# Performance work log

Measured on AMD Instinct MI355X. Metric: run time of the kernel, lower is better.

The kernel has to match this reference:

```python
import jax, jax.numpy as jnp
import numpy as np

D_MODEL, D_K, D_V = 1024, 128, 128
B, S = 4, 4096

def setup_inputs() -> dict:
    key = jax.random.key(0)
    ks = jax.random.split(key, 9)
    sq = 1.0 / np.sqrt(D_MODEL)
    return {
        "q": jax.random.normal(ks[0], (B, S, D_MODEL), jnp.float32),
        "k": jax.random.normal(ks[1], (B, S, D_MODEL), jnp.float32),
        "v": jax.random.normal(ks[2], (B, S, D_MODEL), jnp.float32),
        "wq": jax.random.uniform(ks[3], (D_MODEL, D_K), jnp.float32, -sq, sq),
        "bq": jax.random.uniform(ks[4], (D_K,), jnp.float32, -sq, sq),
        "wk": jax.random.uniform(ks[5], (D_MODEL, D_K), jnp.float32, -sq, sq),
        "bk": jax.random.uniform(ks[6], (D_K,), jnp.float32, -sq, sq),
        "wv": jax.random.uniform(ks[7], (D_MODEL, D_V), jnp.float32, -sq, sq),
        "bv": jax.random.uniform(ks[8], (D_V,), jnp.float32, -sq, sq),
    }

def reference(q, k, v, wq, bq, wk, bk, wv, bv):
    scale = 1.0 / jnp.sqrt(jnp.asarray(D_K, q.dtype))
    qp = q @ wq + bq            # [B,S,Dk]
    kp = k @ wk + bk            # [B,S,Dk]
    vp = v @ wv + bv            # [B,S,Dv]
    scores = jnp.einsum('bqd,bkd->bqk', qp, kp) * scale  # [B,S,S]
    attn = jax.nn.softmax(scores, axis=-1)
    return jnp.einsum('bqk,bkd->bqd', attn, vp)          # [B,S,Dv]
```

## Files before the change

### kernel.cpp

```cpp
#include <hip/hip_runtime.h>

#define DM 1024
#define DK 128
#define SEQ 4096
#define NB 4
#define NSPLIT 4
#define KSPAN (SEQ / NSPLIT)
#define NQT (SEQ / 128)

typedef float f32x4 __attribute__((ext_vector_type(4)));
typedef float f32x16 __attribute__((ext_vector_type(16)));
typedef __bf16 bf16x8 __attribute__((ext_vector_type(8)));
typedef unsigned short u16x8 __attribute__((ext_vector_type(8)));
typedef unsigned short u16x4 __attribute__((ext_vector_type(4)));

__device__ __forceinline__ unsigned short f2bf(float f) {
    unsigned int u = __builtin_bit_cast(unsigned int, f);
    u += 0x7fffu + ((u >> 16) & 1u);
    return (unsigned short)(u >> 16);
}
__device__ __forceinline__ float bf2f(unsigned short h) {
    unsigned int u = ((unsigned int)h) << 16;
    return __builtin_bit_cast(float, u);
}
__device__ __forceinline__ f32x4 mfma16(u16x8 a, u16x8 b, f32x4 c) {
    return __builtin_amdgcn_mfma_f32_16x16x32_bf16(
        __builtin_bit_cast(bf16x8, a), __builtin_bit_cast(bf16x8, b), c, 0, 0, 0);
}
__device__ __forceinline__ f32x16 mfma32(u16x8 a, u16x8 b, f32x16 c) {
    return __builtin_amdgcn_mfma_f32_32x32x16_bf16(
        __builtin_bit_cast(bf16x8, a), __builtin_bit_cast(bf16x8, b), c, 0, 0, 0);
}

__global__ __launch_bounds__(256) void wt_kernel(
        const float* __restrict__ wq, const float* __restrict__ wk,
        const float* __restrict__ wv, unsigned short* __restrict__ wT) {
    __shared__ unsigned short T[64 * 72];
    const int kt = blockIdx.x, dt = blockIdx.y, mat = blockIdx.z;
    const float* src = (mat == 0) ? wq : (mat == 1 ? wk : wv);
    const int tid = threadIdx.x;
    const int rb = tid >> 4, c4 = (tid & 15) * 4;
    float4 x[4];
#pragma unroll
    for (int i = 0; i < 4; i++)
        x[i] = *(const float4*)&src[(size_t)(kt * 64 + i * 16 + rb) * DK + dt * 64 + c4];
#pragma unroll
    for (int i = 0; i < 4; i++) {
        const int row = i * 16 + rb;
        T[(c4 + 0) * 72 + row] = f2bf(x[i].x);
        T[(c4 + 1) * 72 + row] = f2bf(x[i].y);
        T[(c4 + 2) * 72 + row] = f2bf(x[i].z);
        T[(c4 + 3) * 72 + row] = f2bf(x[i].w);
    }
    __syncthreads();
    const int dl = tid >> 2, ks0 = (tid & 3) * 16;
    unsigned short* dst = wT + (size_t)mat * DM * DK + (size_t)(dt * 64 + dl) * DM + kt * 64 + ks0;
#pragma unroll
    for (int j = 0; j < 2; j++)
        *(u16x8*)&dst[8 * j] = *(const u16x8*)&T[dl * 72 + ks0 + 8 * j];
}

__global__ __launch_bounds__(256)
__attribute__((amdgpu_waves_per_eu(3, 3)))
void proj_kernel(
        const float* __restrict__ qin, const float* __restrict__ kin,
        const float* __restrict__ vin, const unsigned short* __restrict__ wT,
        const float* __restrict__ bq, const float* __restrict__ bk,
        const float* __restrict__ bv,
        unsigned short* __restrict__ qp, unsigned short* __restrict__ kp,
        unsigned short* __restrict__ vpT) {
    __shared__ unsigned short Xs[64 * 136];
    __shared__ unsigned short Ws[128 * 136];
    const int y = blockIdx.y;
    const float* X = (y == 0) ? qin : (y == 1 ? kin : vin);
    const unsigned short* WTm = wT + (size_t)y * (DM * DK);
    const float* bias = (y == 0) ? bq : (y == 1 ? bk : bv);

    const int tid = threadIdx.x;
    const int w = tid >> 6, lane = tid & 63, l16 = lane & 15, quad = lane >> 4;
    const int t0 = blockIdx.x * 64;
    const int xr = tid >> 5, xc = (tid & 31) * 4;
    const int wr = tid >> 4, wc = (tid & 15) * 8;

    f32x4 zero = {0.f, 0.f, 0.f, 0.f};
    f32x4 acc[4][2];
#pragma unroll
    for (int mf = 0; mf < 4; mf++)
#pragma unroll
        for (int nf = 0; nf < 2; nf++) acc[mf][nf] = zero;

    float4 xv[8];
    uint4 wv[8];
#pragma unroll
    for (int i = 0; i < 8; i++) {
        xv[i] = *(const float4*)&X[(size_t)(t0 + i * 8 + xr) * DM + xc];
        wv[i] = *(const uint4*)&WTm[(size_t)(i * 16 + wr) * DM + wc];
    }

    for (int k0 = 0; k0 < DM; k0 += 128) {
        __syncthreads();
#pragma unroll
        for (int i = 0; i < 8; i++) {
            u16x4 p;
            p[0] = f2bf(xv[i].x); p[1] = f2bf(xv[i].y);
            p[2] = f2bf(xv[i].z); p[3] = f2bf(xv[i].w);
            *(u16x4*)&Xs[(i * 8 + xr) * 136 + xc] = p;
            *(u16x8*)&Ws[(i * 16 + wr) * 136 + wc] = __builtin_bit_cast(u16x8, wv[i]);
        }
        __syncthreads();
        if (k0 + 128 < DM) {
#pragma unroll
            for (int i = 0; i < 8; i++) {
                xv[i] = *(const float4*)&X[(size_t)(t0 + i * 8 + xr) * DM + (k0 + 128) + xc];
                wv[i] = *(const uint4*)&WTm[(size_t)(i * 16 + wr) * DM + (k0 + 128) + wc];
            }
        }
#pragma unroll
        for (int ks = 0; ks < 4; ks++) {
            u16x8 av[4], bvf[2];
#pragma unroll
            for (int mf = 0; mf < 4; mf++)
                av[mf] = *(const u16x8*)&Xs[(l16 + 16 * mf) * 136 + ks * 32 + quad * 8];
#pragma unroll
            for (int nf = 0; nf < 2; nf++)
                bvf[nf] = *(const u16x8*)&Ws[(l16 + 32 * w + 16 * nf) * 136 + ks * 32 + quad * 8];
#pragma unroll
            for (int mf = 0; mf < 4; mf++)
#pragma unroll
                for (int nf = 0; nf < 2; nf++)
                    acc[mf][nf] = mfma16(av[mf], bvf[nf], acc[mf][nf]);
        }
    }
    if (y < 2) {
        unsigned short* outp = y ? kp : qp;
#pragma unroll
        for (int nf = 0; nf < 2; nf++) {
            const int n = l16 + 32 * w + 16 * nf;
            const float bb = bias[n];
#pragma unroll
            for (int mf = 0; mf < 4; mf++)
#pragma unroll
                for (int r = 0; r < 4; r++)
                    outp[(size_t)(t0 + 16 * mf + quad * 4 + r) * DK + n] = f2bf(acc[mf][nf][r] + bb);
        }
    } else {
        __syncthreads();
        unsigned short* Tb = Ws;
#pragma unroll
        for (int nf = 0; nf < 2; nf++) {
            const int d = l16 + 32 * w + 16 * nf;
            const float bb = bias[d];
#pragma unroll
            for (int mf = 0; mf < 4; mf++)
#pragma unroll
                for (int r = 0; r < 4; r++)
                    Tb[d * 72 + 16 * mf + quad * 4 + r] = f2bf(acc[mf][nf][r] + bb);
        }
        __syncthreads();
        const int d2 = tid >> 1, ts = (tid & 1) * 32;
        const int b2 = t0 >> 12, tl0 = t0 & (SEQ - 1);
#pragma unroll
        for (int j = 0; j < 4; j++)
            *(u16x8*)&vpT[((size_t)(b2 * DK + d2)) * SEQ + tl0 + ts + 8 * j] =
                *(const u16x8*)&Tb[d2 * 72 + ts + 8 * j];
    }
}

__global__ __launch_bounds__(256)
__attribute__((amdgpu_waves_per_eu(2, 2)))
void attn_part_kernel(
        const unsigned short* __restrict__ qp, const unsigned short* __restrict__ kp,
        const unsigned short* __restrict__ vpT,
        unsigned short* __restrict__ Opart, float* __restrict__ Lw) {
    __shared__ unsigned short Ks[64 * 136];
    __shared__ unsigned short Vs[128 * 72];

    const int tid = threadIdx.x;
    const int w = tid >> 6, lane = tid & 63, l32 = lane & 31, h = lane >> 5;
    const int qt = blockIdx.x, pi = blockIdx.y, b = blockIdx.z;
    const int q0 = qt * 128;
    const int kbase = pi * KSPAN;
    const float csc = 0.08838834764831845f * 1.4426950408889634f;

    u16x8 qf[8];
    {
        const unsigned short* qrow = qp + (size_t)(b * SEQ + q0 + 32 * w + l32) * DK + 8 * h;
#pragma unroll
        for (int c = 0; c < 8; c++) qf[c] = *(const u16x8*)&qrow[16 * c];
    }

    f32x16 oacc[4];
#pragma unroll
    for (int i = 0; i < 4; i++)
#pragma unroll
        for (int j = 0; j < 16; j++) oacc[i][j] = 0.f;
    float l_acc = 0.f;

    const int krow = tid >> 2, kch = (tid & 3) * 8;
    const int vrow = tid >> 1, voff = (tid & 1) * 8;
    uint4 kbuf[4], vbuf[4];
    {
        const unsigned short* kg = kp + (size_t)(b * SEQ + kbase + krow) * DK + kch;
        const unsigned short* vg = vpT + (size_t)(b * DK + vrow) * SEQ + kbase + voff;
#pragma unroll
        for (int i = 0; i < 4; i++) {
            kbuf[i] = *(const uint4*)&kg[32 * i];
            vbuf[i] = *(const uint4*)&vg[16 * i];
        }
    }

    for (int it = 0; it < KSPAN / 64; it++) {
        __syncthreads();
#pragma unroll
        for (int i = 0; i < 4; i++) {
            *(u16x8*)&Ks[krow * 136 + kch + 32 * i] = __builtin_bit_cast(u16x8, kbuf[i]);
            *(u16x8*)&Vs[vrow * 72 + voff + 16 * i] = __builtin_bit_cast(u16x8, vbuf[i]);
        }
        __syncthreads();
        if (it + 1 < KSPAN / 64) {
            const int kn = kbase + (it + 1) * 64;
            const unsigned short* kg = kp + (size_t)(b * SEQ + kn + krow) * DK + kch;
            const unsigned short* vg = vpT + (size_t)(b * DK + vrow) * SEQ + kn + voff;
#pragma unroll
            for (int i = 0; i < 4; i++) {
                kbuf[i] = *(const uint4*)&kg[32 * i];
                vbuf[i] = *(const uint4*)&vg[16 * i];
            }
        }
        f32x16 sacc[2];
#pragma unroll
        for (int kb = 0; kb < 2; kb++)
#pragma unroll
            for (int j = 0; j < 16; j++) sacc[kb][j] = 0.f;
#pragma unroll
        for (int c = 0; c < 8; c++)
#pragma unroll
            for (int kb = 0; kb < 2; kb++) {
                u16x8 kf = *(const u16x8*)&Ks[(l32 + 32 * kb) * 136 + 16 * c + 8 * h];
                sacc[kb] = mfma32(kf, qf[c], sacc[kb]);
            }
        unsigned int pp[16];
#pragma unroll
        for (int kb = 0; kb < 2; kb++)
#pragma unroll
            for (int r2 = 0; r2 < 8; r2++) {
                float p0 = exp2f(sacc[kb][2 * r2] * csc);
                float p1 = exp2f(sacc[kb][2 * r2 + 1] * csc);
                l_acc += p0 + p1;
                pp[kb * 8 + r2] = (unsigned int)f2bf(p0) | ((unsigned int)f2bf(p1) << 16);
            }
#pragma unroll
        for (int c = 0; c < 4; c++) {
            const int bs = (c >> 1) * 8 + (c & 1) * 4;
            unsigned int o0 = pp[bs], o1 = pp[bs + 1], o2 = pp[bs + 2], o3 = pp[bs + 3];
            unsigned int x0 = __shfl_xor(o0, 32), x1 = __shfl_xor(o1, 32);
            unsigned int x2 = __shfl_xor(o2, 32), x3 = __shfl_xor(o3, 32);
            uint4 af;
            af.x = h ? x2 : o0;
            af.y = h ? x3 : o1;
            af.z = h ? o2 : x0;
            af.w = h ? o3 : x1;
            u16x8 afr = __builtin_bit_cast(u16x8, af);
#pragma unroll
            for (int db = 0; db < 4; db++) {
                u16x8 vf = *(const u16x8*)&Vs[(32 * db + l32) * 72 + 16 * c + 8 * h];
                oacc[db] = mfma32(afr, vf, oacc[db]);
            }
        }
    }
    float l_tot = l_acc + __shfl_xor(l_acc, 32);
    if (lane < 32)
        Lw[(size_t)(b * NSPLIT + pi) * SEQ + q0 + 32 * w + l32] = l_tot;
    float rl[16];
#pragma unroll
    for (int r = 0; r < 16; r++) {
        int qr = (r & 3) + 8 * (r >> 2) + 4 * h;
        rl[r] = 1.f / __shfl(l_tot, qr);
    }
    unsigned short* ob = Opart + ((size_t)((b * NSPLIT + pi) * NQT + qt)) * 16384 + (size_t)tid * 64;
#pragma unroll
    for (int db = 0; db < 4; db++) {
        u16x8 s0, s1;
#pragma unroll
        for (int j = 0; j < 8; j++) {
            s0[j] = f2bf(oacc[db][j] * rl[j]);
            s1[j] = f2bf(oacc[db][8 + j] * rl[8 + j]);
        }
        *(u16x8*)&ob[db * 16] = s0;
        *(u16x8*)&ob[db * 16 + 8] = s1;
    }
}

__global__ __launch_bounds__(256) void attn_combine_kernel(
        const unsigned short* __restrict__ Opart, const float* __restrict__ Lw,
        float* __restrict__ out) {
    __shared__ float Ls[NSPLIT * 128];
    const int tid = threadIdx.x;
    const int w = tid >> 6, lane = tid & 63, l32 = lane & 31, h = lane >> 5;
    const int qt = blockIdx.x, b = blockIdx.y, z = blockIdx.z;
    const int q0 = qt * 128;
    for (int i = tid; i < NSPLIT * 128; i += 256) {
        int pi = i >> 7, ql = i & 127;
        Ls[i] = Lw[(size_t)(b * NSPLIT + pi) * SEQ + q0 + ql];
    }
    __syncthreads();
    int qlr[16];
    float inv[16];
#pragma unroll
    for (int r = 0; r < 16; r++) {
        qlr[r] = 32 * w + (r & 3) + 8 * (r >> 2) + 4 * h;
        float s = 0.f;
#pragma unroll
        for (int pi = 0; pi < NSPLIT; pi++) s += Ls[pi * 128 + qlr[r]];
        inv[r] = 1.f / s;
    }
    float acc[32];
#pragma unroll
    for (int i = 0; i < 32; i++) acc[i] = 0.f;
#pragma unroll
    for (int pi = 0; pi < NSPLIT; pi++) {
        float wr[16];
#pragma unroll
        for (int r = 0; r < 16; r++) wr[r] = Ls[pi * 128 + qlr[r]] * inv[r];
        const unsigned short* ob =
            Opart + ((size_t)((b * NSPLIT + pi) * NQT + qt)) * 16384 + (size_t)tid * 64;
#pragma unroll
        for (int j = 0; j < 2; j++) {
            const int db = 2 * z + j;
#pragma unroll
            for (int hf = 0; hf < 2; hf++) {
                u16x8 v8 = *(const u16x8*)&ob[db * 16 + 8 * hf];
#pragma unroll
                for (int jj = 0; jj < 8; jj++)
                    acc[j * 16 + 8 * hf + jj] += wr[8 * hf + jj] * bf2f(v8[jj]);
            }
        }
    }
#pragma unroll
    for (int j = 0; j < 2; j++) {
        const int db = 2 * z + j;
#pragma unroll
        for (int r = 0; r < 16; r++)
            out[(size_t)(b * SEQ + q0 + qlr[r]) * DK + 32 * db + l32] = acc[j * 16 + r];
    }
}

extern "C" void kernel_launch(void* const* d_in, const int* in_sizes, int n_in,
                              void* d_out, int out_size, void* d_ws, size_t ws_size,
                              hipStream_t stream) {
    const float* q  = (const float*)d_in[0];
    const float* k  = (const float*)d_in[1];
    const float* v  = (const float*)d_in[2];
    const float* wq = (const float*)d_in[3];
    const float* bq = (const float*)d_in[4];
    const float* wk = (const float*)d_in[5];
    const float* bk = (const float*)d_in[6];
    const float* wv = (const float*)d_in[7];
    const float* bv = (const float*)d_in[8];
    float* out = (float*)d_out;

    char* ws = (char*)d_ws;
    unsigned short* wT    = (unsigned short*)(ws);
    unsigned short* qp    = (unsigned short*)(ws + (1u << 20));
    unsigned short* kpb   = (unsigned short*)(ws + (5u << 20));
    unsigned short* vpT   = (unsigned short*)(ws + (9u << 20));
    unsigned short* Opart = (unsigned short*)(ws + (13u << 20));
    float* Lw             = (float*)(ws + (29u << 20));

    hipLaunchKernelGGL(wt_kernel, dim3(16, 2, 3), dim3(256), 0, stream, wq, wk, wv, wT);
    hipLaunchKernelGGL(proj_kernel, dim3(256, 3), dim3(256), 0, stream,
                       q, k, v, wT, bq, bk, bv, qp, kpb, vpT);
    hipLaunchKernelGGL(attn_part_kernel, dim3(NQT, NSPLIT, NB), dim3(256), 0, stream,
                       qp, kpb, vpT, Opart, Lw);
    hipLaunchKernelGGL(attn_combine_kernel, dim3(NQT, NB, 2), dim3(256), 0, stream,
                       Opart, Lw, out);
}
```

Baseline: 278.3 us.

## Stream projection tiles to LDS via global_load_lds with swizzled layout

Projection GEMM loads now go straight from global memory into LDS with direct-to-LDS 16-byte loads instead of staging through registers. The fp32 X tile is kept as fp32 in an XOR-swizzled LDS layout and converted to bf16 when read for MFMA. The K step drops from 128 to 64 and the waves_per_eu attribute is removed. This saves register staging and store instructions and may raise occupancy, but the next tile's load is issued only after compute, so global latency is no longer hidden behind the MFMAs.

```diff
diff --git a/kernel.cpp b/kernel.cpp
--- a/kernel.cpp
+++ b/kernel.cpp
@@ -1,4 +1,5 @@
 #include <hip/hip_runtime.h>
+#include <stdint.h>
 
 #define DM 1024
 #define DK 128
@@ -30,6 +31,20 @@
 __device__ __forceinline__ f32x16 mfma32(u16x8 a, u16x8 b, f32x16 c) {
     return __builtin_amdgcn_mfma_f32_32x32x16_bf16(
         __builtin_bit_cast(bf16x8, a), __builtin_bit_cast(bf16x8, b), c, 0, 0, 0);
+}
+
+__device__ __forceinline__ bf16x8 cvt84(f32x4 lo, f32x4 hi) {
+    bf16x8 r;
+    r[0] = (__bf16)lo[0]; r[1] = (__bf16)lo[1]; r[2] = (__bf16)lo[2]; r[3] = (__bf16)lo[3];
+    r[4] = (__bf16)hi[0]; r[5] = (__bf16)hi[1]; r[6] = (__bf16)hi[2]; r[7] = (__bf16)hi[3];
+    return r;
+}
+
+__device__ __forceinline__ void gll16(const void* g, void* l) {
+    __builtin_amdgcn_global_load_lds(
+        (const __attribute__((address_space(1))) unsigned int*)(uintptr_t)g,
+        (__attribute__((address_space(3))) unsigned int*)(uintptr_t)l,
+        16, 0, 0);
 }
 
 __global__ __launch_bounds__(256) void wt_kernel(
@@ -61,7 +76,6 @@
 }
 
 __global__ __launch_bounds__(256)
-__attribute__((amdgpu_waves_per_eu(3, 3)))
 void proj_kernel(
         const float* __restrict__ qin, const float* __restrict__ kin,
         const float* __restrict__ vin, const unsigned short* __restrict__ wT,
@@ -69,8 +83,10 @@
         const float* __restrict__ bv,
         unsigned short* __restrict__ qp, unsigned short* __restrict__ kp,
         unsigned short* __restrict__ vpT) {
-    __shared__ unsigned short Xs[64 * 136];
-    __shared__ unsigned short Ws[128 * 136];
+    __shared__ __align__(16) char smem[64 * 64 * 4 + 128 * 64 * 2];
+    float* Xs = (float*)smem;
+    unsigned short* Ws = (unsigned short*)(smem + 64 * 64 * 4);
+
     const int y = blockIdx.y;
     const float* X = (y == 0) ? qin : (y == 1 ? kin : vin);
     const unsigned short* WTm = wT + (size_t)y * (DM * DK);
@@ -79,8 +95,25 @@
     const int tid = threadIdx.x;
     const int w = tid >> 6, lane = tid & 63, l16 = lane & 15, quad = lane >> 4;
     const int t0 = blockIdx.x * 64;
-    const int xr = tid >> 5, xc = (tid & 31) * 4;
-    const int wr = tid >> 4, wc = (tid & 15) * 8;
+
+    const int lr4 = lane >> 4, h16 = lane & 15;
+    const int lr8 = lane >> 3, h8 = lane & 7;
+    const float* xsrc[4];
+    const unsigned short* wsrc[4];
+    float* xdst[4];
+    unsigned short* wdst[4];
+#pragma unroll
+    for (int i = 0; i < 4; i++) {
+        const int xrow = w * 16 + i * 4 + lr4;
+        const int xcol = (((h16 >> 1) ^ (xrow & 7)) << 3) |
+                         (((h16 & 1) ^ ((xrow >> 3) & 1)) << 2);
+        xsrc[i] = X + (size_t)(t0 + xrow) * DM + xcol;
+        xdst[i] = Xs + (w * 16 + i * 4) * 64;
+        const int wrow = w * 32 + i * 8 + lr8;
+        const int wcol = (h8 ^ lr8) << 3;
+        wsrc[i] = WTm + (size_t)wrow * DM + wcol;
+        wdst[i] = Ws + (w * 32 + i * 8) * 64;
+    }
 
     f32x4 zero = {0.f, 0.f, 0.f, 0.f};
     f32x4 acc[4][2];
@@ -89,48 +122,46 @@
 #pragma unroll
         for (int nf = 0; nf < 2; nf++) acc[mf][nf] = zero;
 
-    float4 xv[8];
-    uint4 wv[8];
-#pragma unroll
-    for (int i = 0; i < 8; i++) {
-        xv[i] = *(const float4*)&X[(size_t)(t0 + i * 8 + xr) * DM + xc];
-        wv[i] = *(const uint4*)&WTm[(size_t)(i * 16 + wr) * DM + wc];
-    }
-
-    for (int k0 = 0; k0 < DM; k0 += 128) {
-        __syncthreads();
-#pragma unroll
-        for (int i = 0; i < 8; i++) {
-            u16x4 p;
-            p[0] = f2bf(xv[i].x); p[1] = f2bf(xv[i].y);
-            p[2] = f2bf(xv[i].z); p[3] = f2bf(xv[i].w);
-            *(u16x4*)&Xs[(i * 8 + xr) * 136 + xc] = p;
-            *(u16x8*)&Ws[(i * 16 + wr) * 136 + wc] = __builtin_bit_cast(u16x8, wv[i]);
-        }
-        __syncthreads();
-        if (k0 + 128 < DM) {
-#pragma unroll
-            for (int i = 0; i < 8; i++) {
-                xv[i] = *(const float4*)&X[(size_t)(t0 + i * 8 + xr) * DM + (k0 + 128) + xc];
-                wv[i] = *(const uint4*)&WTm[(size_t)(i * 16 + wr) * DM + (k0 + 128) + wc];
-            }
-        }
-#pragma unroll
-        for (int ks = 0; ks < 4; ks++) {
-            u16x8 av[4], bvf[2];
+#pragma unroll
+    for (int i = 0; i < 4; i++) { gll16(xsrc[i], xdst[i]); gll16(wsrc[i], wdst[i]); }
+
+    const int swz = l16 & 7, h3 = (l16 >> 3) & 1;
+    for (int t = 0; t < 16; ++t) {
+        __syncthreads();
+#pragma unroll
+        for (int ks = 0; ks < 2; ks++) {
+            const int ca = ((ks << 2) | quad) ^ swz;
+            bf16x8 av[4];
+            u16x8 bvf[2];
+#pragma unroll
+            for (int mf = 0; mf < 4; mf++) {
+                const float* ap = &Xs[(l16 + 16 * mf) * 64 + ca * 8];
+                f32x4 lo = *(const f32x4*)(ap + 4 * h3);
+                f32x4 hi = *(const f32x4*)(ap + 4 * (h3 ^ 1));
+                av[mf] = cvt84(lo, hi);
+            }
+#pragma unroll
+            for (int nf = 0; nf < 2; nf++)
+                bvf[nf] = *(const u16x8*)&Ws[(32 * w + 16 * nf + l16) * 64 + ca * 8];
 #pragma unroll
             for (int mf = 0; mf < 4; mf++)
-                av[mf] = *(const u16x8*)&Xs[(l16 + 16 * mf) * 136 + ks * 32 + quad * 8];
-#pragma unroll
-            for (int nf = 0; nf < 2; nf++)
-                bvf[nf] = *(const u16x8*)&Ws[(l16 + 32 * w + 16 * nf) * 136 + ks * 32 + quad * 8];
-#pragma unroll
-            for (int mf = 0; mf < 4; mf++)
 #pragma unroll
                 for (int nf = 0; nf < 2; nf++)
-                    acc[mf][nf] = mfma16(av[mf], bvf[nf], acc[mf][nf]);
-        }
-    }
+                    acc[mf][nf] = __builtin_amdgcn_mfma_f32_16x16x32_bf16(
+                        av[mf], __builtin_bit_cast(bf16x8, bvf[nf]), acc[mf][nf], 0, 0, 0);
+        }
+        __syncthreads();
+        if (t < 15) {
+#pragma unroll
+            for (int i = 0; i < 4; i++) {
+                xsrc[i] += 64;
+                wsrc[i] += 64;
+                gll16(xsrc[i], xdst[i]);
+                gll16(wsrc[i], wdst[i]);
+            }
+        }
+    }
+
     if (y < 2) {
         unsigned short* outp = y ? kp : qp;
 #pragma unroll
@@ -145,7 +176,7 @@
         }
     } else {
         __syncthreads();
-        unsigned short* Tb = Ws;
+        unsigned short* Tb = (unsigned short*)smem;
 #pragma unroll
         for (int nf = 0; nf < 2; nf++) {
             const int d = l16 + 32 * w + 16 * nf;
```

New measurement: 286.9 us. +3.1%, slower.

## Load projection GEMM operands directly from global into MFMA registers, drop LDS staging

Applied to the files above, without the earlier changes.

The projection kernel no longer stages X and W tiles through shared memory. Each lane now loads its MFMA fragments straight from global memory with one-step register prefetch, and converts to bf16 using native casts. Removing the LDS stage and its barriers is meant to cut sync and LDS traffic, and the waves_per_eu cap is dropped. In exchange, each wave reloads X rows that the other waves also need, so the block issues four times the global X reads. The access pattern is also less coalesced (32-byte chunks per lane), and there is no deep pipeline to hide memory latency.

```diff
diff --git a/kernel.cpp b/kernel.cpp
--- a/kernel.cpp
+++ b/kernel.cpp
@@ -1,4 +1,5 @@
 #include <hip/hip_runtime.h>
+#include <stdint.h>
 
 #define DM 1024
 #define DK 128
@@ -23,13 +24,20 @@
     unsigned int u = ((unsigned int)h) << 16;
     return __builtin_bit_cast(float, u);
 }
-__device__ __forceinline__ f32x4 mfma16(u16x8 a, u16x8 b, f32x4 c) {
+__device__ __forceinline__ f32x4 mfma16b(bf16x8 a, u16x8 b, f32x4 c) {
     return __builtin_amdgcn_mfma_f32_16x16x32_bf16(
-        __builtin_bit_cast(bf16x8, a), __builtin_bit_cast(bf16x8, b), c, 0, 0, 0);
+        a, __builtin_bit_cast(bf16x8, b), c, 0, 0, 0);
 }
 __device__ __forceinline__ f32x16 mfma32(u16x8 a, u16x8 b, f32x16 c) {
     return __builtin_amdgcn_mfma_f32_32x32x16_bf16(
         __builtin_bit_cast(bf16x8, a), __builtin_bit_cast(bf16x8, b), c, 0, 0, 0);
+}
+
+__device__ __forceinline__ bf16x8 cvt84(f32x4 lo, f32x4 hi) {
+    bf16x8 r;
+    r[0] = (__bf16)lo[0]; r[1] = (__bf16)lo[1]; r[2] = (__bf16)lo[2]; r[3] = (__bf16)lo[3];
+    r[4] = (__bf16)hi[0]; r[5] = (__bf16)hi[1]; r[6] = (__bf16)hi[2]; r[7] = (__bf16)hi[3];
+    return r;
 }
 
 __global__ __launch_bounds__(256) void wt_kernel(
@@ -61,7 +69,6 @@
 }
 
 __global__ __launch_bounds__(256)
-__attribute__((amdgpu_waves_per_eu(3, 3)))
 void proj_kernel(
         const float* __restrict__ qin, const float* __restrict__ kin,
         const float* __restrict__ vin, const unsigned short* __restrict__ wT,
@@ -69,8 +76,8 @@
         const float* __restrict__ bv,
         unsigned short* __restrict__ qp, unsigned short* __restrict__ kp,
         unsigned short* __restrict__ vpT) {
-    __shared__ unsigned short Xs[64 * 136];
-    __shared__ unsigned short Ws[128 * 136];
+    __shared__ unsigned short Tb[128 * 72];
+
     const int y = blockIdx.y;
     const float* X = (y == 0) ? qin : (y == 1 ? kin : vin);
     const unsigned short* WTm = wT + (size_t)y * (DM * DK);
@@ -79,8 +86,9 @@
     const int tid = threadIdx.x;
     const int w = tid >> 6, lane = tid & 63, l16 = lane & 15, quad = lane >> 4;
     const int t0 = blockIdx.x * 64;
-    const int xr = tid >> 5, xc = (tid & 31) * 4;
-    const int wr = tid >> 4, wc = (tid & 15) * 8;
+
+    const float* xb = X + (size_t)(t0 + l16) * DM + quad * 8;
+    const unsigned short* wb = WTm + (size_t)(32 * w + l16) * DM + quad * 8;
 
     f32x4 zero = {0.f, 0.f, 0.f, 0.f};
     f32x4 acc[4][2];
@@ -89,48 +97,35 @@
 #pragma unroll
         for (int nf = 0; nf < 2; nf++) acc[mf][nf] = zero;
 
-    float4 xv[8];
-    uint4 wv[8];
-#pragma unroll
-    for (int i = 0; i < 8; i++) {
-        xv[i] = *(const float4*)&X[(size_t)(t0 + i * 8 + xr) * DM + xc];
-        wv[i] = *(const uint4*)&WTm[(size_t)(i * 16 + wr) * DM + wc];
-    }
-
-    for (int k0 = 0; k0 < DM; k0 += 128) {
-        __syncthreads();
-#pragma unroll
-        for (int i = 0; i < 8; i++) {
-            u16x4 p;
-            p[0] = f2bf(xv[i].x); p[1] = f2bf(xv[i].y);
-            p[2] = f2bf(xv[i].z); p[3] = f2bf(xv[i].w);
-            *(u16x4*)&Xs[(i * 8 + xr) * 136 + xc] = p;
-            *(u16x8*)&Ws[(i * 16 + wr) * 136 + wc] = __builtin_bit_cast(u16x8, wv[i]);
-        }
-        __syncthreads();
-        if (k0 + 128 < DM) {
-#pragma unroll
-            for (int i = 0; i < 8; i++) {
-                xv[i] = *(const float4*)&X[(size_t)(t0 + i * 8 + xr) * DM + (k0 + 128) + xc];
-                wv[i] = *(const uint4*)&WTm[(size_t)(i * 16 + wr) * DM + (k0 + 128) + wc];
-            }
-        }
-#pragma unroll
-        for (int ks = 0; ks < 4; ks++) {
-            u16x8 av[4], bvf[2];
-#pragma unroll
-            for (int mf = 0; mf < 4; mf++)
-                av[mf] = *(const u16x8*)&Xs[(l16 + 16 * mf) * 136 + ks * 32 + quad * 8];
-#pragma unroll
-            for (int nf = 0; nf < 2; nf++)
-                bvf[nf] = *(const u16x8*)&Ws[(l16 + 32 * w + 16 * nf) * 136 + ks * 32 + quad * 8];
-#pragma unroll
-            for (int mf = 0; mf < 4; mf++)
-#pragma unroll
-                for (int nf = 0; nf < 2; nf++)
-                    acc[mf][nf] = mfma16(av[mf], bvf[nf], acc[mf][nf]);
-        }
-    }
+    f32x4 alo[4], ahi[4];
+#pragma unroll
+    for (int mf = 0; mf < 4; mf++) {
+        const float* p = xb + (size_t)mf * (16 * DM);
+        alo[mf] = *(const f32x4*)p;
+        ahi[mf] = *(const f32x4*)(p + 4);
+    }
+
+    for (int t = 0; t < 32; ++t) {
+        const int kn = (t < 31 ? t + 1 : t) * 32;
+        f32x4 nlo[4], nhi[4];
+#pragma unroll
+        for (int mf = 0; mf < 4; mf++) {
+            const float* p = xb + (size_t)mf * (16 * DM) + kn;
+            nlo[mf] = *(const f32x4*)p;
+            nhi[mf] = *(const f32x4*)(p + 4);
+        }
+        u16x8 bv0 = *(const u16x8*)(wb + t * 32);
+        u16x8 bv1 = *(const u16x8*)(wb + 16 * DM + t * 32);
+#pragma unroll
+        for (int mf = 0; mf < 4; mf++) {
+            bf16x8 av = cvt84(alo[mf], ahi[mf]);
+            acc[mf][0] = mfma16b(av, bv0, acc[mf][0]);
+            acc[mf][1] = mfma16b(av, bv1, acc[mf][1]);
+        }
+#pragma unroll
+        for (int mf = 0; mf < 4; mf++) { alo[mf] = nlo[mf]; ahi[mf] = nhi[mf]; }
+    }
+
     if (y < 2) {
         unsigned short* outp = y ? kp : qp;
 #pragma unroll
@@ -144,8 +139,6 @@
                     outp[(size_t)(t0 + 16 * mf + quad * 4 + r) * DK + n] = f2bf(acc[mf][nf][r] + bb);
         }
     } else {
-        __syncthreads();
-        unsigned short* Tb = Ws;
 #pragma unroll
         for (int nf = 0; nf < 2; nf++) {
             const int d = l16 + 32 * w + 16 * nf;
```

Result: slower. 333.4 us (+19.8%).
